# Optimization experiments

Measured on AMD Instinct MI355X. Metric: run time of the kernel, lower is better.

Reference implementation:

```python
import jax, jax.numpy as jnp
import numpy as np

H = 8   # num_heads
K = 7   # kernel_size


def setup_inputs() -> dict:
    key = jax.random.key(0)
    k1, k2, k3 = jax.random.split(key, 3)
    T, B, C = 2048, 16, 512
    x = jax.random.normal(k1, (T, B, C), dtype=jnp.float32)
    query = jax.random.normal(k2, (T, B, C), dtype=jnp.float32)
    W = jax.random.normal(k3, (C, H * K), dtype=jnp.float32) * 0.02
    return {"x": x, "query": query, "W": W}


def reference(x, query, W):
    T, B, C = x.shape
    R = C // H
    # per-position, per-head kernel weights: Dense(H*K) on query, no bias
    weight = jnp.einsum('tbc,cn->tbn', query, W).reshape(T * B * H, K)
    weight = jax.nn.softmax(weight, axis=-1)  # weight_softmax=True; dropout rate 0 is identity
    # TF extract_patches with SAME padding along T: total pad K-1, more on the bottom
    pad_before = (K - 1) // 2
    pad_after = K - 1 - pad_before
    x_pad = jnp.pad(x, ((pad_before, pad_after), (0, 0), (0, 0)))
    idx = jnp.arange(T)[:, None] + jnp.arange(K)[None, :]  # (T, K)
    patches = x_pad[idx]                      # (T, K, B, C)
    patches = jnp.transpose(patches, (0, 2, 1, 3))  # (T, B, K, C): TF depth order is (k, c)
    # Faithful to the source: flat (K*C) axis reinterpreted as (H, R, K)
    x_unfold = patches.reshape(T * B * H, R, K)
    out = jnp.einsum('nrk,nk->nr', x_unfold, weight)  # batched tiny matmul
    return out.reshape(T, B, C)
```

## Files before the change

kernel.cpp:

```cpp
#include <hip/hip_runtime.h>

#define T_DIM 2048
#define B_DIM 16
#define C_DIM 512
#define NW 56

#define A_BYTES  16384
#define XS_OFF   A_BYTES
#define XS_BYTES (22 * 512 * 2)
#define WT_OFF   (A_BYTES + XS_BYTES)
#define F_LDS    (WT_OFF + 16 * NW * 4)

typedef __attribute__((ext_vector_type(8))) short short8;
typedef __attribute__((ext_vector_type(4))) float floatx4;

static __device__ __forceinline__ unsigned short f2bf(float x_) {
    union { float f; unsigned u; } v; v.f = x_;
    return (unsigned short)((v.u + 0x7FFFu + ((v.u >> 16) & 1u)) >> 16);
}
static __device__ __forceinline__ float bf_lo(unsigned u) {
    union { unsigned u; float f; } c; c.u = u << 16; return c.f;
}
static __device__ __forceinline__ float bf_hi(unsigned u) {
    union { unsigned u; float f; } c; c.u = u & 0xFFFF0000u; return c.f;
}
static __device__ __forceinline__ int swz(int a) { return a ^ ((a >> 3) & 0x70); }
static __device__ __forceinline__ int aswz(int a) {
    return a ^ ((((a >> 8) ^ (a >> 11)) & 7) << 4);
}

__global__ __launch_bounds__(256)
void pack_w(const float* __restrict__ W, short8* __restrict__ Bg) {
    const int g  = blockIdx.x * 256 + threadIdx.x;
    const int ks = g >> 8;
    const int nt = (g >> 6) & 3;
    const int l  = g & 63;
    const int c  = l & 15;
    const int n  = nt * 14 + c;
    const int k0 = ks * 32 + ((l >> 4) & 3) * 8;
    short8 o;
#pragma unroll
    for (int j = 0; j < 8; ++j) {
        const float v = (c < 14) ? W[(size_t)(k0 + j) * NW + n] : 0.f;
        o[j] = (short)f2bf(v);
    }
    Bg[g] = o;
}

__global__ __launch_bounds__(512, 6)
void fused3(const float* __restrict__ x, const float* __restrict__ q,
            const short8* __restrict__ Bg, float* __restrict__ out) {
    __shared__ __align__(16) char S[F_LDS];

    const int tid  = threadIdx.x;
    const int lane = tid & 63;
    const int wv   = tid >> 6;
    const int b    = blockIdx.x & 15;
    const int t0   = (blockIdx.x >> 4) * 16;

    float4 qr[4];
#pragma unroll
    for (int j = 0; j < 4; ++j) {
        const int idx = tid + j * 512;
        const int r   = idx >> 7;
        const int cc  = (idx & 127) * 4;
        qr[j] = *(const float4*)(q + ((size_t)(t0 + r) * B_DIM + b) * C_DIM + cc);
    }
    float4 xr[6];
#pragma unroll
    for (int j = 0; j < 6; ++j) {
        const int idx = tid + j * 512;
        xr[j] = make_float4(0.f, 0.f, 0.f, 0.f);
        if (idx < 2816) {
            const int i  = idx >> 7;
            const int cc = (idx & 127) * 4;
            const int tp = t0 + i - 3;
            if (tp >= 0 && tp < T_DIM)
                xr[j] = *(const float4*)(x + ((size_t)tp * B_DIM + b) * C_DIM + cc);
        }
    }

    char* AS = S;
#pragma unroll
    for (int j = 0; j < 4; ++j) {
        const int idx = tid + j * 512;
        const int r   = idx >> 7;
        const int cc  = (idx & 127) * 4;
        const int a   = (cc >> 5) * 1024 + ((cc >> 3) & 3) * 256 + r * 16 +
                        (cc & 7) * 2;
        uint2 p;
        p.x = (unsigned)f2bf(qr[j].x) | ((unsigned)f2bf(qr[j].y) << 16);
        p.y = (unsigned)f2bf(qr[j].z) | ((unsigned)f2bf(qr[j].w) << 16);
        *(uint2*)(AS + aswz(a)) = p;
    }
    char* XS = S + XS_OFF;
#pragma unroll
    for (int j = 0; j < 6; ++j) {
        const int idx = tid + j * 512;
        if (idx < 2816) {
            uint2 p;
            p.x = (unsigned)f2bf(xr[j].x) | ((unsigned)f2bf(xr[j].y) << 16);
            p.y = (unsigned)f2bf(xr[j].z) | ((unsigned)f2bf(xr[j].w) << 16);
            *(uint2*)(XS + swz(idx * 8)) = p;
        }
    }
    __syncthreads();

    float* wt = (float*)(S + WT_OFF);
    if (wv < 4) {
        floatx4 acc = (floatx4){0.f, 0.f, 0.f, 0.f};
#pragma unroll
        for (int ks = 0; ks < 16; ++ks) {
            const short8 af = *(const short8*)(AS + aswz(ks * 1024 + lane * 16));
            const short8 bf = Bg[(ks * 4 + wv) * 64 + lane];
            acc = __builtin_amdgcn_mfma_f32_16x16x32_bf16(af, bf, acc, 0, 0, 0);
        }
        const int c    = lane & 15;
        const int cb   = (c < 7) ? 0 : 7;
        const int sb   = (lane & 48) + cb;
        const int quad = lane >> 4;
#pragma unroll
        for (int r = 0; r < 4; ++r) {
            const float a = acc[r];
            const float v0 = __shfl(a, sb + 0);
            const float v1 = __shfl(a, sb + 1);
            const float v2 = __shfl(a, sb + 2);
            const float v3 = __shfl(a, sb + 3);
            const float v4 = __shfl(a, sb + 4);
            const float v5 = __shfl(a, sb + 5);
            const float v6 = __shfl(a, sb + 6);
            const float mx = fmaxf(fmaxf(fmaxf(v0, v1), fmaxf(v2, v3)),
                                   fmaxf(fmaxf(v4, v5), v6));
            const float sm = __expf(v0 - mx) + __expf(v1 - mx) + __expf(v2 - mx) +
                             __expf(v3 - mx) + __expf(v4 - mx) + __expf(v5 - mx) +
                             __expf(v6 - mx);
            const float w = __expf(a - mx) * (1.0f / sm);
            if (c < 14)
                wt[(quad * 4 + r) * NW + wv * 14 + c] = w;
        }
    }
    __syncthreads();

    const int h = lane >> 3;
    const int base_b = lane * 112;
#pragma unroll
    for (int s = 0; s < 2; ++s) {
        const int tt = wv * 2 + s;
        const int tb = tt * 1024 + base_b;
        uint4 xu[7];
#pragma unroll
        for (int i = 0; i < 7; ++i)
            xu[i] = *(const uint4*)(XS + swz(tb + i * 16));
        float xf[56];
#pragma unroll
        for (int i = 0; i < 7; ++i) {
            xf[i * 8 + 0] = bf_lo(xu[i].x); xf[i * 8 + 1] = bf_hi(xu[i].x);
            xf[i * 8 + 2] = bf_lo(xu[i].y); xf[i * 8 + 3] = bf_hi(xu[i].y);
            xf[i * 8 + 4] = bf_lo(xu[i].z); xf[i * 8 + 5] = bf_hi(xu[i].z);
            xf[i * 8 + 6] = bf_lo(xu[i].w); xf[i * 8 + 7] = bf_hi(xu[i].w);
        }
        const float* wp = wt + tt * NW + h * 7;
        float w[7];
#pragma unroll
        for (int k = 0; k < 7; ++k) w[k] = wp[k];
        float a8[8];
#pragma unroll
        for (int r = 0; r < 8; ++r) {
            float sacc = xf[r * 7] * w[0];
#pragma unroll
            for (int k = 1; k < 7; ++k) sacc = fmaf(w[k], xf[r * 7 + k], sacc);
            a8[r] = sacc;
        }
        float* orow = out + ((size_t)(t0 + tt) * B_DIM + b) * C_DIM + lane * 8;
        *(float4*)(orow)     = make_float4(a8[0], a8[1], a8[2], a8[3]);
        *(float4*)(orow + 4) = make_float4(a8[4], a8[5], a8[6], a8[7]);
    }
}

extern "C" void kernel_launch(void* const* d_in, const int* in_sizes, int n_in,
                              void* d_out, int out_size, void* d_ws, size_t ws_size,
                              hipStream_t stream) {
    const float* x = (const float*)d_in[0];
    const float* q = (const float*)d_in[1];
    const float* W = (const float*)d_in[2];
    float* out = (float*)d_out;
    short8* Bg = (short8*)d_ws;

    pack_w<<<16, 256, 0, stream>>>(W, Bg);
    fused3<<<(T_DIM / 16) * B_DIM, 512, 0, stream>>>(x, q, Bg, out);
}
```

Before: 176.0 us.

## Warp-specialize q and x loads so x staging overlaps the MFMA softmax

Splits the block so waves 0-3 load and convert q, then run the MFMA projection and softmax, while waves 4-7 load x and write the bf16 x tile to LDS concurrently. The softmax weight table now reuses the q buffer's LDS region, which shrinks the LDS footprint, and launch bounds are raised to allow more resident blocks. The MFMA chain is split into two accumulators to shorten the dependency chain. In exchange it adds an extra barrier, and x-loading waves now hold 11 float4 registers each.

```diff
diff --git a/kernel.cpp b/kernel.cpp
--- a/kernel.cpp
+++ b/kernel.cpp
@@ -5,11 +5,9 @@
 #define C_DIM 512
 #define NW 56
 
-#define A_BYTES  16384
-#define XS_OFF   A_BYTES
+#define XS_OFF   16384
 #define XS_BYTES (22 * 512 * 2)
-#define WT_OFF   (A_BYTES + XS_BYTES)
-#define F_LDS    (WT_OFF + 16 * NW * 4)
+#define F_LDS    (XS_OFF + XS_BYTES)
 
 typedef __attribute__((ext_vector_type(8))) short short8;
 typedef __attribute__((ext_vector_type(4))) float floatx4;
@@ -47,8 +45,8 @@
     Bg[g] = o;
 }
 
-__global__ __launch_bounds__(512, 6)
-void fused3(const float* __restrict__ x, const float* __restrict__ q,
+__global__ __launch_bounds__(512, 8)
+void fused4(const float* __restrict__ x, const float* __restrict__ q,
             const short8* __restrict__ Bg, float* __restrict__ out) {
     __shared__ __align__(16) char S[F_LDS];
 
@@ -58,67 +56,65 @@
     const int b    = blockIdx.x & 15;
     const int t0   = (blockIdx.x >> 4) * 16;
 
-    float4 qr[4];
-#pragma unroll
-    for (int j = 0; j < 4; ++j) {
-        const int idx = tid + j * 512;
-        const int r   = idx >> 7;
-        const int cc  = (idx & 127) * 4;
-        qr[j] = *(const float4*)(q + ((size_t)(t0 + r) * B_DIM + b) * C_DIM + cc);
-    }
-    float4 xr[6];
-#pragma unroll
-    for (int j = 0; j < 6; ++j) {
-        const int idx = tid + j * 512;
-        xr[j] = make_float4(0.f, 0.f, 0.f, 0.f);
-        if (idx < 2816) {
-            const int i  = idx >> 7;
-            const int cc = (idx & 127) * 4;
-            const int tp = t0 + i - 3;
+    char*  AS = S;
+    char*  XS = S + XS_OFF;
+    float* wt = (float*)S;
+
+    float4 xr[11];
+    const int xtid = tid - 256;
+
+    if (wv < 4) {
+        float4 qr[8];
+#pragma unroll
+        for (int j = 0; j < 8; ++j) {
+            const int idx = tid + j * 256;
+            const int r   = idx >> 7;
+            const int cc  = (idx & 127) * 4;
+            qr[j] = *(const float4*)(q + ((size_t)(t0 + r) * B_DIM + b) * C_DIM + cc);
+        }
+#pragma unroll
+        for (int j = 0; j < 8; ++j) {
+            const int idx = tid + j * 256;
+            const int r   = idx >> 7;
+            const int cc  = (idx & 127) * 4;
+            const int a   = (cc >> 5) * 1024 + ((cc >> 3) & 3) * 256 + r * 16 +
+                            (cc & 7) * 2;
+            uint2 p;
+            p.x = (unsigned)f2bf(qr[j].x) | ((unsigned)f2bf(qr[j].y) << 16);
+            p.y = (unsigned)f2bf(qr[j].z) | ((unsigned)f2bf(qr[j].w) << 16);
+            *(uint2*)(AS + aswz(a)) = p;
+        }
+    } else {
+#pragma unroll
+        for (int j = 0; j < 11; ++j) {
+            const int idx = xtid + j * 256;
+            const int i   = idx >> 7;
+            const int cc  = (idx & 127) * 4;
+            const int tp  = t0 + i - 3;
+            xr[j] = make_float4(0.f, 0.f, 0.f, 0.f);
             if (tp >= 0 && tp < T_DIM)
                 xr[j] = *(const float4*)(x + ((size_t)tp * B_DIM + b) * C_DIM + cc);
         }
     }
-
-    char* AS = S;
-#pragma unroll
-    for (int j = 0; j < 4; ++j) {
-        const int idx = tid + j * 512;
-        const int r   = idx >> 7;
-        const int cc  = (idx & 127) * 4;
-        const int a   = (cc >> 5) * 1024 + ((cc >> 3) & 3) * 256 + r * 16 +
-                        (cc & 7) * 2;
-        uint2 p;
-        p.x = (unsigned)f2bf(qr[j].x) | ((unsigned)f2bf(qr[j].y) << 16);
-        p.y = (unsigned)f2bf(qr[j].z) | ((unsigned)f2bf(qr[j].w) << 16);
-        *(uint2*)(AS + aswz(a)) = p;
-    }
-    char* XS = S + XS_OFF;
-#pragma unroll
-    for (int j = 0; j < 6; ++j) {
-        const int idx = tid + j * 512;
-        if (idx < 2816) {
-            uint2 p;
-            p.x = (unsigned)f2bf(xr[j].x) | ((unsigned)f2bf(xr[j].y) << 16);
-            p.y = (unsigned)f2bf(xr[j].z) | ((unsigned)f2bf(xr[j].w) << 16);
-            *(uint2*)(XS + swz(idx * 8)) = p;
-        }
-    }
     __syncthreads();
 
-    float* wt = (float*)(S + WT_OFF);
+    float wres[4];
     if (wv < 4) {
-        floatx4 acc = (floatx4){0.f, 0.f, 0.f, 0.f};
-#pragma unroll
-        for (int ks = 0; ks < 16; ++ks) {
-            const short8 af = *(const short8*)(AS + aswz(ks * 1024 + lane * 16));
-            const short8 bf = Bg[(ks * 4 + wv) * 64 + lane];
-            acc = __builtin_amdgcn_mfma_f32_16x16x32_bf16(af, bf, acc, 0, 0, 0);
-        }
-        const int c    = lane & 15;
-        const int cb   = (c < 7) ? 0 : 7;
-        const int sb   = (lane & 48) + cb;
-        const int quad = lane >> 4;
+        floatx4 acc0 = (floatx4){0.f, 0.f, 0.f, 0.f};
+        floatx4 acc1 = (floatx4){0.f, 0.f, 0.f, 0.f};
+#pragma unroll
+        for (int ks = 0; ks < 16; ks += 2) {
+            const short8 af0 = *(const short8*)(AS + aswz(ks * 1024 + lane * 16));
+            const short8 bf0 = Bg[(ks * 4 + wv) * 64 + lane];
+            acc0 = __builtin_amdgcn_mfma_f32_16x16x32_bf16(af0, bf0, acc0, 0, 0, 0);
+            const short8 af1 = *(const short8*)(AS + aswz((ks + 1) * 1024 + lane * 16));
+            const short8 bf1 = Bg[((ks + 1) * 4 + wv) * 64 + lane];
+            acc1 = __builtin_amdgcn_mfma_f32_16x16x32_bf16(af1, bf1, acc1, 0, 0, 0);
+        }
+        const floatx4 acc = acc0 + acc1;
+        const int c  = lane & 15;
+        const int cb = (c < 7) ? 0 : 7;
+        const int sb = (lane & 48) + cb;
 #pragma unroll
         for (int r = 0; r < 4; ++r) {
             const float a = acc[r];
@@ -134,9 +130,27 @@
             const float sm = __expf(v0 - mx) + __expf(v1 - mx) + __expf(v2 - mx) +
                              __expf(v3 - mx) + __expf(v4 - mx) + __expf(v5 - mx) +
                              __expf(v6 - mx);
-            const float w = __expf(a - mx) * (1.0f / sm);
-            if (c < 14)
-                wt[(quad * 4 + r) * NW + wv * 14 + c] = w;
+            wres[r] = __expf(a - mx) * (1.0f / sm);
+        }
+    } else {
+#pragma unroll
+        for (int j = 0; j < 11; ++j) {
+            const int idx = xtid + j * 256;
+            uint2 p;
+            p.x = (unsigned)f2bf(xr[j].x) | ((unsigned)f2bf(xr[j].y) << 16);
+            p.y = (unsigned)f2bf(xr[j].z) | ((unsigned)f2bf(xr[j].w) << 16);
+            *(uint2*)(XS + swz(idx * 8)) = p;
+        }
+    }
+    __syncthreads();
+
+    if (wv < 4) {
+        const int c    = lane & 15;
+        const int quad = lane >> 4;
+        if (c < 14) {
+#pragma unroll
+            for (int r = 0; r < 4; ++r)
+                wt[(quad * 4 + r) * NW + wv * 14 + c] = wres[r];
         }
     }
     __syncthreads();
@@ -187,5 +201,5 @@
     short8* Bg = (short8*)d_ws;
 
     pack_w<<<16, 256, 0, stream>>>(W, Bg);
-    fused3<<<(T_DIM / 16) * B_DIM, 512, 0, stream>>>(x, q, Bg, out);
-}
+    fused4<<<(T_DIM / 16) * B_DIM, 512, 0, stream>>>(x, q, Bg, out);
+}
```

After: 175.5 us. Within noise of the previous version (-0.3%).
